# Kernel optimization log

Hardware: AMD Instinct MI355X
Metric: run time of the kernel (lower is better)

## Reference

```python
import jax, jax.numpy as jnp
import numpy as np
import math

V = 1_000_000   # vocabulary / item count
D = 64          # embedding dim
B = 128         # batch
N = 50          # max_len (targets per user)
K = 1024        # noise_ratio
NORM_TERM = math.log(V)   # norm_term='auto' -> log(noise.numel())
LOG_K = math.log(K)


def setup_inputs() -> dict:
    key = jax.random.key(0)
    k1, k2, k3, k4 = jax.random.split(key, 4)
    target = jax.random.randint(k1, (B, N), 0, V)
    inp = jax.random.normal(k2, (B, N, D), dtype=jnp.float32)
    embs = jax.random.normal(k3, (V, D), dtype=jnp.float32) * 0.02
    # per_word=False: one shared draw of K noise item ids (alias-table sample)
    noise_samples = jax.random.randint(k4, (K,), 0, V)
    # uniform noise distribution, clamped + renormalized then logged
    logprob_noise = jnp.full((V,), -math.log(V), dtype=jnp.float32)
    return {"target": target, "input": inp, "embs": embs,
            "noise_samples": noise_samples, "logprob_noise": logprob_noise}


def _bce_with_logits(x, y):
    # numerically stable BCEWithLogitsLoss (reduction='none')
    return jnp.maximum(x, 0.0) - x * y + jnp.log1p(jnp.exp(-jnp.abs(x)))


def reference(target, input, embs, noise_samples, logprob_noise):
    # --- noise log-probs (irregular gathers over huge table) ---
    logit_noise_in_noise = logprob_noise[noise_samples]          # [K]
    logit_target_in_noise = logprob_noise[target]                # [B,N]
    # --- model scores (get_score) ---
    tgt_emb = embs[target]                                        # [B,N,D] gather
    target_score = jnp.einsum('bnd,bnd->bn', input, tgt_emb)      # [B,N]
    noise_emb = embs[noise_samples]                               # [K,D] gather
    noise_score = jnp.einsum('bnd,kd->bnk', input, noise_emb)     # [B,N,K]
    # --- _get_logit: subtract lnZ ---
    logit_target_in_model = target_score - NORM_TERM
    logit_noise_in_model = noise_score - NORM_TERM
    # --- nce_loss ---
    logits = jnp.concatenate([logit_target_in_model[..., None],
                              logit_noise_in_model], axis=-1)     # [B,N,K+1]
    q_logits = jnp.concatenate(
        [logit_target_in_noise[..., None],
         jnp.broadcast_to(logit_noise_in_noise, (B, N, K))], axis=-1)
    x = logits - q_logits - LOG_K                                 # [B,N,K+1]
    labels = jnp.zeros((B, N, K + 1), dtype=x.dtype).at[..., 0].set(1.0)
    loss = _bce_with_logits(x, labels).sum(axis=-1)               # [B,N]
    # reduction='elementwise_mean'
    return loss.mean()
```

## Files before the change

### kernel.cpp

```cpp
#include <hip/hip_runtime.h>
#include <math.h>

#define DIM 64
#define TILE 64

__global__ __launch_bounds__(256) void nce_target_kernel(
    const float* __restrict__ inp, const float* __restrict__ embs,
    const int* __restrict__ tgt, const float* __restrict__ lpn,
    float cadd, float* __restrict__ partials)
{
    int tid = threadIdx.x;
    int wave = tid >> 6, lane = tid & 63;
    int r = blockIdx.x * 4 + wave;
    int t = tgt[r];
    float a = inp[(size_t)r * DIM + lane];
    float e = embs[(size_t)t * DIM + lane];
    float p = a * e;
    #pragma unroll
    for (int off = 32; off > 0; off >>= 1) p += __shfl_xor(p, off);
    __shared__ float red[4];
    if (lane == 0) {
        float x0 = p + cadd - lpn[t];
        red[wave] = fmaxf(x0, 0.f) - x0 + log1pf(__expf(-fabsf(x0)));
    }
    __syncthreads();
    if (tid == 0) partials[blockIdx.x] = red[0] + red[1] + red[2] + red[3];
}

__global__ __launch_bounds__(256) void nce_noise_kernel(
    const float* __restrict__ inp, const float* __restrict__ embs,
    const int* __restrict__ ns, const float* __restrict__ lpn,
    float cadd, int nColTiles, float* __restrict__ partials)
{
    __shared__ float As[DIM][TILE + 4];
    __shared__ float Bs[DIM][TILE + 4];
    __shared__ float cks[TILE];
    __shared__ float red[4];

    int tid = threadIdx.x;
    int rowTile = blockIdx.x / nColTiles;
    int colTile = blockIdx.x % nColTiles;
    int rBase = rowTile * TILE;
    int cBase = colTile * TILE;

    const float4* Ag4 = (const float4*)(inp + (size_t)rBase * DIM);
    #pragma unroll
    for (int c = 0; c < 4; ++c) {
        int f = c * 256 + tid;
        int row = f >> 4;
        int dq = f & 15;
        float4 v = Ag4[f];
        As[dq*4+0][row] = v.x; As[dq*4+1][row] = v.y;
        As[dq*4+2][row] = v.z; As[dq*4+3][row] = v.w;
    }
    #pragma unroll
    for (int c = 0; c < 4; ++c) {
        int f = c * 256 + tid;
        int col = f >> 4;
        int dq = f & 15;
        int item = ns[cBase + col];
        float4 v = ((const float4*)(embs + (size_t)item * DIM))[dq];
        Bs[dq*4+0][col] = v.x; Bs[dq*4+1][col] = v.y;
        Bs[dq*4+2][col] = v.z; Bs[dq*4+3][col] = v.w;
    }
    if (tid < TILE) cks[tid] = cadd - lpn[ns[cBase + tid]];
    __syncthreads();

    int tx = tid & 15, ty = tid >> 4;
    float acc[4][4] = {};
    #pragma unroll 16
    for (int d = 0; d < DIM; ++d) {
        float4 a = *(const float4*)&As[d][ty * 4];
        float4 b = *(const float4*)&Bs[d][tx * 4];
        float av[4] = {a.x, a.y, a.z, a.w};
        float bv[4] = {b.x, b.y, b.z, b.w};
        #pragma unroll
        for (int i = 0; i < 4; ++i)
            #pragma unroll
            for (int j = 0; j < 4; ++j)
                acc[i][j] = fmaf(av[i], bv[j], acc[i][j]);
    }

    float s = 0.f;
    #pragma unroll
    for (int i = 0; i < 4; ++i)
        #pragma unroll
        for (int j = 0; j < 4; ++j) {
            float x = acc[i][j] + cks[tx * 4 + j];
            s += fmaxf(x, 0.f) + log1pf(__expf(-fabsf(x)));
        }

    #pragma unroll
    for (int off = 32; off > 0; off >>= 1) s += __shfl_xor(s, off);
    int wave = tid >> 6, lane = tid & 63;
    if (lane == 0) red[wave] = s;
    __syncthreads();
    if (tid == 0) partials[blockIdx.x] = red[0] + red[1] + red[2] + red[3];
}

__global__ __launch_bounds__(256) void nce_finalize_kernel(
    const float* __restrict__ partials, int n, float invRows, float* __restrict__ out)
{
    int tid = threadIdx.x;
    float s = 0.f;
    for (int i = tid; i < n; i += 256) s += partials[i];
    #pragma unroll
    for (int off = 32; off > 0; off >>= 1) s += __shfl_xor(s, off);
    __shared__ float red[4];
    int wave = tid >> 6, lane = tid & 63;
    if (lane == 0) red[wave] = s;
    __syncthreads();
    if (tid == 0) out[0] = (red[0] + red[1] + red[2] + red[3]) * invRows;
}

extern "C" void kernel_launch(void* const* d_in, const int* in_sizes, int n_in,
                              void* d_out, int out_size, void* d_ws, size_t ws_size,
                              hipStream_t stream) {
    const int*   target = (const int*)d_in[0];
    const float* input  = (const float*)d_in[1];
    const float* embs   = (const float*)d_in[2];
    const int*   ns     = (const int*)d_in[3];
    const float* lpn    = (const float*)d_in[4];
    float* out = (float*)d_out;

    int nRows = in_sizes[0];
    int K     = in_sizes[3];
    long long V = in_sizes[4];
    float NORM = logf((float)V);
    float LOGK = logf((float)K);
    float cadd = -(NORM + LOGK);

    float* ws = (float*)d_ws;
    int nRowTiles = nRows / TILE;
    int nColTiles = K / TILE;
    int nMain = nRowTiles * nColTiles;
    int nTgtBlocks = nRows / 4;
    float* pMain = ws;
    float* pTgt  = ws + nMain;

    nce_target_kernel<<<nTgtBlocks, 256, 0, stream>>>(input, embs, target, lpn, cadd, pTgt);
    nce_noise_kernel<<<nMain, 256, 0, stream>>>(input, embs, ns, lpn, cadd, nColTiles, pMain);
    nce_finalize_kernel<<<1, 256, 0, stream>>>(ws, nMain + nTgtBlocks,
                                               1.0f / (float)nRows, out);
}
```

Measured before the change: 336.9 us.

## Fuse target-score kernel into noise GEMM kernel and use fast softplus

The separate target-score kernel is folded into the main noise tile kernel: blocks with column tile zero also compute the 64 target dot products and their BCE terms before loading the GEMM tiles. This removes one launch and shrinks the partial-sum buffer the finalize kernel reduces. The softplus also switches from log1pf to __logf(1+exp), a cheaper but slightly less accurate form that adds rounding error for large |z|. Blocks in column tile zero do more work than the others, which slightly unbalances the grid.

```diff
diff --git a/kernel.cpp b/kernel.cpp
--- a/kernel.cpp
+++ b/kernel.cpp
@@ -4,33 +4,15 @@
 #define DIM 64
 #define TILE 64
 
-__global__ __launch_bounds__(256) void nce_target_kernel(
-    const float* __restrict__ inp, const float* __restrict__ embs,
-    const int* __restrict__ tgt, const float* __restrict__ lpn,
-    float cadd, float* __restrict__ partials)
-{
-    int tid = threadIdx.x;
-    int wave = tid >> 6, lane = tid & 63;
-    int r = blockIdx.x * 4 + wave;
-    int t = tgt[r];
-    float a = inp[(size_t)r * DIM + lane];
-    float e = embs[(size_t)t * DIM + lane];
-    float p = a * e;
-    #pragma unroll
-    for (int off = 32; off > 0; off >>= 1) p += __shfl_xor(p, off);
-    __shared__ float red[4];
-    if (lane == 0) {
-        float x0 = p + cadd - lpn[t];
-        red[wave] = fmaxf(x0, 0.f) - x0 + log1pf(__expf(-fabsf(x0)));
-    }
-    __syncthreads();
-    if (tid == 0) partials[blockIdx.x] = red[0] + red[1] + red[2] + red[3];
+__device__ __forceinline__ float softplus_fast(float z) {
+    return fmaxf(z, 0.f) + __logf(1.f + __expf(-fabsf(z)));
 }
 
-__global__ __launch_bounds__(256) void nce_noise_kernel(
+__global__ __launch_bounds__(256) void nce_main_kernel(
     const float* __restrict__ inp, const float* __restrict__ embs,
-    const int* __restrict__ ns, const float* __restrict__ lpn,
-    float cadd, int nColTiles, float* __restrict__ partials)
+    const int* __restrict__ tgt, const int* __restrict__ ns,
+    const float* __restrict__ lpn, float cadd, int nColTiles,
+    float* __restrict__ partials)
 {
     __shared__ float As[DIM][TILE + 4];
     __shared__ float Bs[DIM][TILE + 4];
@@ -42,6 +24,28 @@
     int colTile = blockIdx.x % nColTiles;
     int rBase = rowTile * TILE;
     int cBase = colTile * TILE;
+
+    float s = 0.f;
+
+    if (colTile == 0) {
+        int r4 = tid >> 2, q = tid & 3;
+        int row = rBase + r4;
+        int t = tgt[row];
+        const float4* er = (const float4*)(embs + (size_t)t * DIM) + q * 4;
+        const float4* ir = (const float4*)(inp + (size_t)row * DIM) + q * 4;
+        float p = 0.f;
+        #pragma unroll
+        for (int j = 0; j < 4; ++j) {
+            float4 e = er[j]; float4 a = ir[j];
+            p += a.x * e.x + a.y * e.y + a.z * e.z + a.w * e.w;
+        }
+        p += __shfl_xor(p, 1);
+        p += __shfl_xor(p, 2);
+        if (q == 0) {
+            float x0 = p + cadd - lpn[t];
+            s += softplus_fast(-x0);
+        }
+    }
 
     const float4* Ag4 = (const float4*)(inp + (size_t)rBase * DIM);
     #pragma unroll
@@ -81,14 +85,11 @@
                 acc[i][j] = fmaf(av[i], bv[j], acc[i][j]);
     }
 
-    float s = 0.f;
     #pragma unroll
     for (int i = 0; i < 4; ++i)
         #pragma unroll
-        for (int j = 0; j < 4; ++j) {
-            float x = acc[i][j] + cks[tx * 4 + j];
-            s += fmaxf(x, 0.f) + log1pf(__expf(-fabsf(x)));
-        }
+        for (int j = 0; j < 4; ++j)
+            s += softplus_fast(acc[i][j] + cks[tx * 4 + j]);
 
     #pragma unroll
     for (int off = 32; off > 0; off >>= 1) s += __shfl_xor(s, off);
@@ -134,12 +135,8 @@
     int nRowTiles = nRows / TILE;
     int nColTiles = K / TILE;
     int nMain = nRowTiles * nColTiles;
-    int nTgtBlocks = nRows / 4;
-    float* pMain = ws;
-    float* pTgt  = ws + nMain;
 
-    nce_target_kernel<<<nTgtBlocks, 256, 0, stream>>>(input, embs, target, lpn, cadd, pTgt);
-    nce_noise_kernel<<<nMain, 256, 0, stream>>>(input, embs, ns, lpn, cadd, nColTiles, pMain);
-    nce_finalize_kernel<<<1, 256, 0, stream>>>(ws, nMain + nTgtBlocks,
-                                               1.0f / (float)nRows, out);
+    nce_main_kernel<<<nMain, 256, 0, stream>>>(input, embs, target, ns, lpn,
+                                               cadd, nColTiles, ws);
+    nce_finalize_kernel<<<1, 256, 0, stream>>>(ws, nMain, 1.0f / (float)nRows, out);
 }
```

Result: faster. 316.2 us (-6.2%).
